# Kernel optimization log

Hardware: AMD Instinct MI355X
Metric: run time of the kernel (lower is better)

The kernel has to match this reference:

```python
import jax, jax.numpy as jnp
import numpy as np

NEG_SLOPE = 0.2

def _gat_layer(x, src, dst, W, a_src, a_dst, bias, concat):
    # x: [N, F_in]; W: [F_in, H*C]; a_src/a_dst: [H, C]; bias: [H*C] or [C]
    N = x.shape[0]
    H, C = a_src.shape
    h = (x @ W).reshape(N, H, C)                      # node features per head
    e_src = jnp.einsum('nhc,hc->nh', h, a_src)        # [N, H]
    e_dst = jnp.einsum('nhc,hc->nh', h, a_dst)        # [N, H]
    e = jax.nn.leaky_relu(e_src[src] + e_dst[dst], NEG_SLOPE)  # [E, H]
    # segment softmax over incoming edges of each destination node
    m = jax.ops.segment_max(e, dst, num_segments=N)   # [N, H]
    p = jnp.exp(e - m[dst])
    denom = jax.ops.segment_sum(p, dst, num_segments=N)
    alpha = p / denom[dst]                            # [E, H]
    msg = h[src] * alpha[:, :, None]                  # [E, H, C]
    out = jax.ops.segment_sum(msg, dst, num_segments=N)  # [N, H, C]
    if concat:
        out = out.reshape(N, H * C) + bias
    else:
        out = out.mean(axis=1) + bias
    return out, alpha


def setup_inputs() -> dict:
    key = jax.random.key(0)
    ks = jax.random.split(key, 12)
    N, E = 20000, 320000
    F_in, Ch, Co, H = 256, 64, 64, 8
    x = jax.random.normal(ks[0], (N, F_in), dtype=jnp.float32)
    edge_index = jax.random.randint(ks[1], (2, E), 0, N, dtype=jnp.int64)
    s = 0.05
    return {
        'x': x,
        'edge_index': edge_index,
        'W1': jax.random.normal(ks[2], (F_in, H * Ch), dtype=jnp.float32) * s,
        'att_src1': jax.random.normal(ks[3], (H, Ch), dtype=jnp.float32) * s,
        'att_dst1': jax.random.normal(ks[4], (H, Ch), dtype=jnp.float32) * s,
        'b1': jnp.zeros((H * Ch,), dtype=jnp.float32),
        'W2': jax.random.normal(ks[5], (H * Ch, H * Co), dtype=jnp.float32) * s,
        'att_src2': jax.random.normal(ks[6], (H, Co), dtype=jnp.float32) * s,
        'att_dst2': jax.random.normal(ks[7], (H, Co), dtype=jnp.float32) * s,
        'b2': jnp.zeros((Co,), dtype=jnp.float32),
    }


def reference(x, edge_index, W1, att_src1, att_dst1, b1, W2, att_src2, att_dst2, b2):
    N = x.shape[0]
    # PyG GATConv adds self-loops by default
    loop = jnp.arange(N, dtype=edge_index.dtype)
    src = jnp.concatenate([edge_index[0], loop])
    dst = jnp.concatenate([edge_index[1], loop])
    h1, alpha1 = _gat_layer(x, src, dst, W1, att_src1, att_dst1, b1, concat=True)
    h1 = jax.nn.relu(h1)
    h2, alpha2 = _gat_layer(h1, src, dst, W2, att_src2, att_dst2, b2, concat=False)
    return h2, alpha1, alpha2
```

## Files before the change

kernel.cpp:

```cpp
#include <hip/hip_runtime.h>

#define H 8
#define C 64
#define HC 512
#define NEG 0.2f

typedef __attribute__((ext_vector_type(8))) _Float16 half8v;
typedef __attribute__((ext_vector_type(4))) _Float16 half4v;
typedef __attribute__((ext_vector_type(4))) float f32x4;

__device__ __forceinline__ float leaky(float x) { return x > 0.f ? x : NEG * x; }

#define GLOAD_LDS16(gp, lp) \
  __builtin_amdgcn_global_load_lds((const __attribute__((address_space(1))) unsigned int*)(gp), \
                                   (__attribute__((address_space(3))) unsigned int*)(lp), 16, 0, 0)

__global__ void k_degree(const int* __restrict__ ei, int E, int N, int* __restrict__ deg) {
    int e = blockIdx.x * blockDim.x + threadIdx.x;
    int Et = E + N;
    if (e >= Et) return;
    int d = (e < E) ? ei[E + e] : (e - E);
    atomicAdd(&deg[d], 1);
}

__global__ __launch_bounds__(1024) void k_scan(const int* __restrict__ deg, int N, int* __restrict__ row_start) {
    __shared__ int part[1024];
    int t = threadIdx.x;
    int chunk = (N + 1023) >> 10;
    int lo = t * chunk, hi = min(lo + chunk, N);
    int s = 0;
    for (int i = lo; i < hi; ++i) s += deg[i];
    part[t] = s;
    __syncthreads();
    for (int off = 1; off < 1024; off <<= 1) {
        int v = (t >= off) ? part[t - off] : 0;
        __syncthreads();
        part[t] += v;
        __syncthreads();
    }
    int base = (t == 0) ? 0 : part[t - 1];
    for (int i = lo; i < hi; ++i) { row_start[i] = base; base += deg[i]; }
    if (t == 1023) row_start[N] = part[1023];
}

__global__ void k_fill(const int* __restrict__ ei, int E, int N,
                       const int* __restrict__ row_start, int* __restrict__ cursor,
                       int* __restrict__ csr_src, int* __restrict__ csr_eid) {
    int e = blockIdx.x * blockDim.x + threadIdx.x;
    int Et = E + N;
    if (e >= Et) return;
    int d, s;
    if (e < E) { s = ei[e]; d = ei[E + e]; } else { s = e - E; d = s; }
    int pos = atomicAdd(&cursor[d], 1);
    int idx = row_start[d] + pos;
    csr_src[idx] = s;
    csr_eid[idx] = e;
}

__global__ void k_tofp16(const float* __restrict__ in, _Float16* __restrict__ out, int n4) {
    int i = blockIdx.x * blockDim.x + threadIdx.x;
    if (i >= n4) return;
    float4 v = reinterpret_cast<const float4*>(in)[i];
    half4v h;
    h[0] = (_Float16)v.x; h[1] = (_Float16)v.y;
    h[2] = (_Float16)v.z; h[3] = (_Float16)v.w;
    reinterpret_cast<half4v*>(out)[i] = h;
}

__global__ void k_tsplit(const float* __restrict__ W, _Float16* __restrict__ th,
                         _Float16* __restrict__ tl, int K, int Nc) {
    int idx = blockIdx.x * blockDim.x + threadIdx.x;
    if (idx >= K * Nc) return;
    int c = idx / K, k = idx - c * K;
    float v = W[(long)k * Nc + c];
    _Float16 hh = (_Float16)v;
    th[idx] = hh;
    tl[idx] = (_Float16)(v - (float)hh);
}

__global__ __launch_bounds__(256) void k_gemm_mfma(const _Float16* __restrict__ A,
                                                   const _Float16* __restrict__ Bh,
                                                   const _Float16* __restrict__ Bl,
                                                   _Float16* __restrict__ Cc, int M, int K, int Pb,
                                                   const float* __restrict__ a_src, const float* __restrict__ a_dst,
                                                   float* __restrict__ e_src, float* __restrict__ e_dst) {
    __shared__ _Float16 lA[4096], lBh[4096], lBl[4096];
    int bid = blockIdx.x;
    int panel = ((bid >> 5) << 3) + (bid & 7);
    int colb  = (bid >> 3) & 3;
    if (panel >= Pb) return;
    int tid = threadIdx.x;
    int w = tid >> 6, lane = tid & 63;
    int wr = w >> 1, wc = w & 1;
    int r0 = panel * 128, c0 = colb * 128;
    f32x4 acc[4][4] = {};
    int frag_off = ((lane >> 4) * 16 + (lane & 15)) * 8;

    for (int k0 = 0; k0 < K; k0 += 32) {
        __syncthreads();
        #pragma unroll
        for (int it = 0; it < 2; ++it) {
            int slot = it * 256 + tid;
            int rb = slot >> 6, kc = (slot >> 4) & 3, r16 = slot & 15;
            long ga = (long)(r0 + rb * 16 + r16) * K + k0 + kc * 8;
            long gb = (long)(c0 + rb * 16 + r16) * K + k0 + kc * 8;
            int ldst = (it * 256 + w * 64) * 8;
            GLOAD_LDS16(A + ga, lA + ldst);
            GLOAD_LDS16(Bh + gb, lBh + ldst);
            GLOAD_LDS16(Bl + gb, lBl + ldst);
        }
        __syncthreads();
        half8v fa[4], fbh[4], fbl[4];
        #pragma unroll
        for (int m = 0; m < 4; ++m) {
            int sa = (wr * 4 + m) * 512 + frag_off;
            fa[m] = *reinterpret_cast<half8v*>(&lA[sa]);
            int sb = (wc * 4 + m) * 512 + frag_off;
            fbh[m] = *reinterpret_cast<half8v*>(&lBh[sb]);
            fbl[m] = *reinterpret_cast<half8v*>(&lBl[sb]);
        }
        #pragma unroll
        for (int m = 0; m < 4; ++m)
            #pragma unroll
            for (int n = 0; n < 4; ++n) {
                acc[m][n] = __builtin_amdgcn_mfma_f32_16x16x32_f16(fa[m], fbh[n], acc[m][n], 0, 0, 0);
                acc[m][n] = __builtin_amdgcn_mfma_f32_16x16x32_f16(fa[m], fbl[n], acc[m][n], 0, 0, 0);
            }
    }
    int head = colb * 2 + wc;
    #pragma unroll
    for (int m = 0; m < 4; ++m)
        #pragma unroll
        for (int j = 0; j < 4; ++j) {
            int gr = r0 + wr * 64 + m * 16 + (lane >> 4) * 4 + j;
            if (gr < M) {
                #pragma unroll
                for (int n = 0; n < 4; ++n)
                    Cc[(long)gr * HC + head * 64 + n * 16 + (lane & 15)] = (_Float16)acc[m][n][j];
            }
        }
    float asv[4], adv[4];
    #pragma unroll
    for (int nn = 0; nn < 4; ++nn) {
        asv[nn] = a_src[head * 64 + nn * 16 + (lane & 15)];
        adv[nn] = a_dst[head * 64 + nn * 16 + (lane & 15)];
    }
    #pragma unroll
    for (int m = 0; m < 4; ++m)
        #pragma unroll
        for (int j = 0; j < 4; ++j) {
            int gr = r0 + wr * 64 + m * 16 + (lane >> 4) * 4 + j;
            float es = 0.f, ed = 0.f;
            #pragma unroll
            for (int nn = 0; nn < 4; ++nn) {
                es = fmaf(acc[m][nn][j], asv[nn], es);
                ed = fmaf(acc[m][nn][j], adv[nn], ed);
            }
            #pragma unroll
            for (int o = 1; o < 16; o <<= 1) {
                es += __shfl_xor(es, o);
                ed += __shfl_xor(ed, o);
            }
            if ((lane & 15) == 0 && gr < M) {
                e_src[gr * 8 + head] = es;
                e_dst[gr * 8 + head] = ed;
            }
        }
}

__global__ __launch_bounds__(512) void k_agg(const half8v* __restrict__ hp8,
                                             const float* __restrict__ e_src,
                                             const float* __restrict__ e_dst,
                                             const int* __restrict__ row_start,
                                             const int* __restrict__ csr_src,
                                             const int* __restrict__ csr_eid,
                                             const float* __restrict__ bias,
                                             float* __restrict__ h2out,
                                             _Float16* __restrict__ h1,
                                             float* __restrict__ alpha,
                                             int N, int concat) {
    __shared__ float pbuf[8][512];
    __shared__ int   sibuf[8][64];
    __shared__ int   eibuf[8][64];
    int wid = threadIdx.x >> 6, lane = threadIdx.x & 63;
    int n = blockIdx.x * 8 + wid;
    if (n >= N) return;
    int lo3 = lane & 7, hi3 = lane >> 3;
    int row = row_start[n];
    int deg = row_start[n + 1] - row;
    int chunks = (deg + 7) >> 3;
    bool small = (deg <= 64);
    float* pw = &pbuf[wid][0];
    float ed = e_dst[n * 8 + lo3];
    float psum = 0.f;
    int idx0 = row + min(lo3, deg - 1);
    int sraw = csr_src[idx0];
    int eidr = csr_eid[idx0];
    for (int c = 0; c < chunks; ++c) {
        int sraw_c = sraw, eidr_c = eidr;
        if (c + 1 < chunks) {
            int idxn = row + min((c + 1) * 8 + lo3, deg - 1);
            sraw = csr_src[idxn];
            eidr = csr_eid[idxn];
        }
        if (small) { sibuf[wid][c * 8 + lo3] = sraw_c; eibuf[wid][c * 8 + lo3] = eidr_c; }
        int sv = __shfl(sraw_c, hi3);
        float es = e_src[sv * 8 + lo3];
        float p = __expf(leaky(es + ed));
        if (c * 8 + hi3 >= deg) p = 0.f;
        psum += p;
        if (small) pw[c * 64 + lane] = p;
    }
    psum += __shfl_xor(psum, 8);
    psum += __shfl_xor(psum, 16);
    psum += __shfl_xor(psum, 32);
    float inv = 1.0f / psum;
    float acc[8] = {};
    for (int c = 0; c < chunks; ++c) {
        float p; int sraw_c, eidr_c;
        if (small) {
            sraw_c = sibuf[wid][c * 8 + lo3];
            eidr_c = eibuf[wid][c * 8 + lo3];
            p = pw[c * 64 + lane];
        } else {
            int idx = row + min(c * 8 + lo3, deg - 1);
            sraw_c = csr_src[idx];
            eidr_c = csr_eid[idx];
            int sv = __shfl(sraw_c, hi3);
            float es = e_src[sv * 8 + lo3];
            p = __expf(leaky(es + ed));
            if (c * 8 + hi3 >= deg) p = 0.f;
        }
        int eid = __shfl(eidr_c, hi3);
        if (c * 8 + hi3 < deg)
            alpha[(long)eid * 8 + lo3] = p * inv;
        #pragma unroll
        for (int eg = 0; eg < 8; ++eg) {
            float pe = __shfl(p, eg * 8 + hi3);
            int   se = __shfl(sraw_c, eg);
            half8v hv = hp8[(long)se * 64 + lane];
            #pragma unroll
            for (int k = 0; k < 8; ++k)
                acc[k] = fmaf((float)hv[k], pe, acc[k]);
        }
    }
    float invg = __shfl(inv, hi3);
    if (concat) {
        const float4* b4 = reinterpret_cast<const float4*>(bias);
        float4 ba = b4[lane * 2], bb = b4[lane * 2 + 1];
        float bv[8] = {ba.x, ba.y, ba.z, ba.w, bb.x, bb.y, bb.z, bb.w};
        half8v hh;
        #pragma unroll
        for (int k = 0; k < 8; ++k) {
            float v = fmaf(acc[k], invg, bv[k]);
            v = v > 0.f ? v : 0.f;
            hh[k] = (_Float16)v;
        }
        reinterpret_cast<half8v*>(h1)[(long)n * 64 + lane] = hh;
    } else {
        float sc = invg * 0.125f;
        #pragma unroll
        for (int k = 0; k < 8; ++k) acc[k] *= sc;
        #pragma unroll
        for (int o = 8; o <= 32; o <<= 1)
            #pragma unroll
            for (int k = 0; k < 8; ++k)
                acc[k] += __shfl_xor(acc[k], o);
        if (hi3 == 0) {
            float4 r0, r1;
            r0.x = acc[0] + bias[lo3 * 8 + 0];
            r0.y = acc[1] + bias[lo3 * 8 + 1];
            r0.z = acc[2] + bias[lo3 * 8 + 2];
            r0.w = acc[3] + bias[lo3 * 8 + 3];
            r1.x = acc[4] + bias[lo3 * 8 + 4];
            r1.y = acc[5] + bias[lo3 * 8 + 5];
            r1.z = acc[6] + bias[lo3 * 8 + 6];
            r1.w = acc[7] + bias[lo3 * 8 + 7];
            float4* o4 = reinterpret_cast<float4*>(h2out + (long)n * 64 + lo3 * 8);
            o4[0] = r0;
            o4[1] = r1;
        }
    }
}

extern "C" void kernel_launch(void* const* d_in, const int* in_sizes, int n_in,
                              void* d_out, int out_size, void* d_ws, size_t ws_size,
                              hipStream_t stream) {
    const float* x   = (const float*)d_in[0];
    const int*   ei  = (const int*)d_in[1];
    const float* W1  = (const float*)d_in[2];
    const float* as1 = (const float*)d_in[3];
    const float* ad1 = (const float*)d_in[4];
    const float* b1  = (const float*)d_in[5];
    const float* W2  = (const float*)d_in[6];
    const float* as2 = (const float*)d_in[7];
    const float* ad2 = (const float*)d_in[8];
    const float* b2  = (const float*)d_in[9];

    int N  = in_sizes[0] / 256;
    int E  = in_sizes[1] / 2;
    int Et = E + N;
    int K1 = 256;
    int Mb   = (N + 127) / 128;
    int Mpad = Mb * 128;

    float* out    = (float*)d_out;
    float* h2_out = out;
    float* alpha1 = out + (size_t)N * 64;
    float* alpha2 = alpha1 + (size_t)Et * H;

    _Float16* hpre = (_Float16*)d_ws;
    _Float16* h1   = hpre + (size_t)Mpad * HC;
    _Float16* xh   = h1 + (size_t)Mpad * HC;
    _Float16* W1th = xh + (size_t)Mpad * K1;
    _Float16* W1tl = W1th + (size_t)HC * K1;
    _Float16* W2th = W1tl + (size_t)HC * K1;
    _Float16* W2tl = W2th + (size_t)HC * HC;
    float* eS     = (float*)(W2tl + (size_t)HC * HC);
    float* eD     = eS + (size_t)N * H;
    int*   deg    = (int*)(eD + (size_t)N * H);
    int*   cursor = deg + N;
    int*   row_st = cursor + N;
    int*   csr_src= row_st + N + 1;
    int*   csr_eid= csr_src + Et;

    hipMemsetAsync(deg, 0, (size_t)2 * N * sizeof(int), stream);
    int tb = 256;
    k_degree<<<(Et + tb - 1) / tb, tb, 0, stream>>>(ei, E, N, deg);
    k_scan<<<1, 1024, 0, stream>>>(deg, N, row_st);
    k_fill<<<(Et + tb - 1) / tb, tb, 0, stream>>>(ei, E, N, row_st, cursor, csr_src, csr_eid);

    int n4 = N * K1 / 4;
    k_tofp16<<<(n4 + tb - 1) / tb, tb, 0, stream>>>(x, xh, n4);
    k_tsplit<<<(K1 * HC + tb - 1) / tb, tb, 0, stream>>>(W1, W1th, W1tl, K1, HC);
    k_tsplit<<<(HC * HC + tb - 1) / tb, tb, 0, stream>>>(W2, W2th, W2tl, HC, HC);

    int Pb8 = ((Mb + 7) / 8) * 8;
    int ggemm = Pb8 * 4;
    int gagg = (N + 7) / 8;
    k_gemm_mfma<<<ggemm, 256, 0, stream>>>(xh, W1th, W1tl, hpre, N, K1, Mb, as1, ad1, eS, eD);
    k_agg<<<gagg, 512, 0, stream>>>((const half8v*)hpre, eS, eD, row_st, csr_src, csr_eid,
                                    b1, nullptr, h1, alpha1, N, 1);
    k_gemm_mfma<<<ggemm, 256, 0, stream>>>(h1, W2th, W2tl, hpre, N, HC, Mb, as2, ad2, eS, eD);
    k_agg<<<gagg, 512, 0, stream>>>((const half8v*)hpre, eS, eD, row_st, csr_src, csr_eid,
                                    b2, h2_out, nullptr, alpha2, N, 0);
}
```

Before: 274.7 us.

## Double-buffer LDS tiles in MFMA GEMM to overlap loads with compute

```diff
diff --git a/kernel.cpp b/kernel.cpp
--- a/kernel.cpp
+++ b/kernel.cpp
@@ -84,7 +84,7 @@
                                                    _Float16* __restrict__ Cc, int M, int K, int Pb,
                                                    const float* __restrict__ a_src, const float* __restrict__ a_dst,
                                                    float* __restrict__ e_src, float* __restrict__ e_dst) {
-    __shared__ _Float16 lA[4096], lBh[4096], lBl[4096];
+    __shared__ _Float16 lA[8192], lBh[8192], lBl[8192];
     int bid = blockIdx.x;
     int panel = ((bid >> 5) << 3) + (bid & 7);
     int colb  = (bid >> 3) & 3;
@@ -96,26 +96,38 @@
     f32x4 acc[4][4] = {};
     int frag_off = ((lane >> 4) * 16 + (lane & 15)) * 8;
 
-    for (int k0 = 0; k0 < K; k0 += 32) {
-        __syncthreads();
-        #pragma unroll
-        for (int it = 0; it < 2; ++it) {
-            int slot = it * 256 + tid;
-            int rb = slot >> 6, kc = (slot >> 4) & 3, r16 = slot & 15;
-            long ga = (long)(r0 + rb * 16 + r16) * K + k0 + kc * 8;
-            long gb = (long)(c0 + rb * 16 + r16) * K + k0 + kc * 8;
-            int ldst = (it * 256 + w * 64) * 8;
-            GLOAD_LDS16(A + ga, lA + ldst);
-            GLOAD_LDS16(Bh + gb, lBh + ldst);
-            GLOAD_LDS16(Bl + gb, lBl + ldst);
-        }
-        __syncthreads();
+    int rb0 = tid >> 6, kc0 = (tid >> 4) & 3, r16_0 = tid & 15;
+    int rb1 = (256 + tid) >> 6, kc1 = ((256 + tid) >> 4) & 3;
+    long gaBase0 = (long)(r0 + rb0 * 16 + r16_0) * K + kc0 * 8;
+    long gbBase0 = (long)(c0 + rb0 * 16 + r16_0) * K + kc0 * 8;
+    long gaBase1 = (long)(r0 + rb1 * 16 + r16_0) * K + kc1 * 8;
+    long gbBase1 = (long)(c0 + rb1 * 16 + r16_0) * K + kc1 * 8;
+    int ldst0 = (w * 64) * 8;
+    int ldst1 = (256 + w * 64) * 8;
+
+#define STAGE(buf, k0)  do { \
+        int off = (buf) * 4096; \
+        GLOAD_LDS16(A  + gaBase0 + (k0), lA  + off + ldst0); \
+        GLOAD_LDS16(Bh + gbBase0 + (k0), lBh + off + ldst0); \
+        GLOAD_LDS16(Bl + gbBase0 + (k0), lBl + off + ldst0); \
+        GLOAD_LDS16(A  + gaBase1 + (k0), lA  + off + ldst1); \
+        GLOAD_LDS16(Bh + gbBase1 + (k0), lBh + off + ldst1); \
+        GLOAD_LDS16(Bl + gbBase1 + (k0), lBl + off + ldst1); \
+    } while (0)
+
+    int nk = K >> 5;
+    STAGE(0, 0);
+    __syncthreads();
+    int cur = 0;
+    for (int t = 0; t < nk; ++t) {
+        if (t + 1 < nk) STAGE(cur ^ 1, (t + 1) * 32);
+        int off = cur * 4096;
         half8v fa[4], fbh[4], fbl[4];
         #pragma unroll
         for (int m = 0; m < 4; ++m) {
-            int sa = (wr * 4 + m) * 512 + frag_off;
+            int sa = off + (wr * 4 + m) * 512 + frag_off;
             fa[m] = *reinterpret_cast<half8v*>(&lA[sa]);
-            int sb = (wc * 4 + m) * 512 + frag_off;
+            int sb = off + (wc * 4 + m) * 512 + frag_off;
             fbh[m] = *reinterpret_cast<half8v*>(&lBh[sb]);
             fbl[m] = *reinterpret_cast<half8v*>(&lBl[sb]);
         }
@@ -126,7 +138,11 @@
                 acc[m][n] = __builtin_amdgcn_mfma_f32_16x16x32_f16(fa[m], fbh[n], acc[m][n], 0, 0, 0);
                 acc[m][n] = __builtin_amdgcn_mfma_f32_16x16x32_f16(fa[m], fbl[n], acc[m][n], 0, 0, 0);
             }
-    }
+        __syncthreads();
+        cur ^= 1;
+    }
+#undef STAGE
+
     int head = colb * 2 + wc;
     #pragma unroll
     for (int m = 0; m < 4; ++m)
```

Result: faster. 258.8 us (-5.8%).
